# Kernel optimization log

Measured on AMD Instinct MI355X. Metric: run time of the kernel, lower is better.

Reference implementation:

```python
import jax, jax.numpy as jnp
import numpy as np

NEG_SLOPE = 0.2  # PyG GATConv default


def setup_inputs() -> dict:
    key = jax.random.key(0)
    k1, k2, k3, k4, k5, k6 = jax.random.split(key, 6)
    N, F_in, F_out, E = 50000, 512, 256, 400000
    x = jax.random.normal(k1, (N, F_in), dtype=jnp.float32)
    adj = jax.random.randint(k2, (2, E), 0, N, dtype=jnp.int64)  # [2, E] edge_index (src, dst)
    glorot = lambda k, shape: jax.random.uniform(
        k, shape, jnp.float32, -1.0, 1.0) * np.sqrt(6.0 / (shape[0] + shape[-1]))
    W = glorot(k3, (F_in, F_out))
    att_src = glorot(k4, (F_out,))
    att_dst = glorot(k5, (F_out,))
    bias = jnp.zeros((F_out,), dtype=jnp.float32)
    return {"x": x, "adj": adj, "W": W, "att_src": att_src, "att_dst": att_dst, "bias": bias}


def reference(x, adj, W, att_src, att_dst, bias):
    N = x.shape[0]
    # add self loops (PyG GATConv default add_self_loops=True)
    loops = jnp.arange(N, dtype=adj.dtype)
    src = jnp.concatenate([adj[0], loops])
    dst = jnp.concatenate([adj[1], loops])

    h = x @ W                          # [N, F_out] projected features
    a_src = h @ att_src                # [N] per-node source attention term
    a_dst = h @ att_dst                # [N]
    e = a_src[src] + a_dst[dst]        # [E+N] edge logits
    e = jnp.where(e > 0, e, NEG_SLOPE * e)  # leaky_relu

    # per-destination softmax over incoming edges (numerically stable)
    m = jax.ops.segment_max(e, dst, num_segments=N)
    ex = jnp.exp(e - m[dst])
    denom = jax.ops.segment_sum(ex, dst, num_segments=N)
    alpha = ex / denom[dst]            # [E+N]

    # weighted scatter-aggregate of source messages
    out = jax.ops.segment_sum(alpha[:, None] * h[src], dst, num_segments=N)
    out = out + bias
    return jax.nn.relu(out)
```

## Files before the change

### kernel.cpp

```cpp
#include <hip/hip_runtime.h>
#include <hip/hip_bf16.h>

typedef __attribute__((ext_vector_type(8))) short bf16x8;
typedef __attribute__((ext_vector_type(4))) float f32x4;
typedef unsigned short u16;

#define F_IN 512
#define F_OUT 256
#define NEG_SLOPE 0.2f

__device__ __forceinline__ float leaky(float e) { return e > 0.f ? e : NEG_SLOPE * e; }

__device__ __forceinline__ u16 f2bf(float x) {
    __hip_bfloat16 h = __float2bfloat16(x);
    return *reinterpret_cast<u16*>(&h);
}
__device__ __forceinline__ void bf2x2(unsigned p, float& a, float& b) {
    a = __uint_as_float(p << 16);
    b = __uint_as_float(p & 0xffff0000u);
}

__device__ __forceinline__ void dma16(const void* g, void* l) {
    __builtin_amdgcn_global_load_lds((const __attribute__((address_space(1))) void*)g,
                                     (__attribute__((address_space(3))) void*)l, 16, 0, 0);
}

__global__ void k_transpose(const float* __restrict__ W, u16* __restrict__ Wt) {
    int t = blockIdx.x * 256 + threadIdx.x;
    int k = t >> 8;
    int n = t & 255;
    Wt[n * F_IN + k] = f2bf(W[k * F_OUT + n]);
}

__global__ __launch_bounds__(256) void k_gemm(const float* __restrict__ X,
                                              const u16* __restrict__ Wt,
                                              u16* __restrict__ Hb, int N) {
    __shared__ float sA[128 * 32];
    __shared__ u16 sB[128 * 32];
    const int tid = threadIdx.x;
    const int wave = tid >> 6, lane = tid & 63;
    const int wm = (wave >> 1) * 64, wn = (wave & 1) * 64;
    const int tile_m = blockIdx.y * 128, tile_n = blockIdx.x * 128;

    f32x4 acc[4][4];
#pragma unroll
    for (int i = 0; i < 4; i++)
#pragma unroll
        for (int j = 0; j < 4; j++) acc[i][j] = (f32x4){0.f, 0.f, 0.f, 0.f};

    const int a_row_in = lane >> 3;
    const int a_gc = (lane & 7) ^ a_row_in;
    const int b_row_in = lane >> 2;
    const int b_gc = (lane & 3) ^ ((lane >> 3) & 3);

    for (int kb = 0; kb < F_IN / 32; ++kb) {
#pragma unroll
        for (int t = 0; t < 4; ++t) {
            int r0 = wave * 32 + t * 8;
            int grow = tile_m + r0 + a_row_in;
            if (grow >= N) grow = N - 1;
            dma16(&X[(size_t)grow * F_IN + kb * 32 + a_gc * 4], &sA[r0 * 32]);
        }
#pragma unroll
        for (int t = 0; t < 2; ++t) {
            int r0 = wave * 32 + t * 16;
            int grow = tile_n + r0 + b_row_in;
            dma16(&Wt[(size_t)grow * F_IN + kb * 32 + b_gc * 8], &sB[r0 * 32]);
        }
        __syncthreads();

        const int lm = lane & 15, q = lane >> 4;
        bf16x8 af[4], bfr[4];
#pragma unroll
        for (int i = 0; i < 4; i++) {
            const int arow = wm + i * 16 + lm;
            const int s7 = arow & 7;
            const float4 c0 = *(const float4*)&sA[arow * 32 + (((2 * q) ^ s7) << 2)];
            const float4 c1 = *(const float4*)&sA[arow * 32 + (((2 * q + 1) ^ s7) << 2)];
            u16 a8[8] = {f2bf(c0.x), f2bf(c0.y), f2bf(c0.z), f2bf(c0.w),
                         f2bf(c1.x), f2bf(c1.y), f2bf(c1.z), f2bf(c1.w)};
            af[i] = *(const bf16x8*)a8;
            const int brow = wn + i * 16 + lm;
            bfr[i] = *(const bf16x8*)&sB[brow * 32 + ((q ^ ((lm >> 1) & 3)) << 3)];
        }
#pragma unroll
        for (int i = 0; i < 4; i++)
#pragma unroll
            for (int j = 0; j < 4; j++)
                acc[i][j] = __builtin_amdgcn_mfma_f32_16x16x32_bf16(af[i], bfr[j], acc[i][j], 0, 0, 0);
        __syncthreads();
    }

    const int lc = lane & 15, lr4 = (lane >> 4) * 4;
    for (int i = 0; i < 4; i++)
        for (int j = 0; j < 4; j++) {
#pragma unroll
            for (int r = 0; r < 4; r++) {
                int row = tile_m + wm + i * 16 + lr4 + r;
                int col = tile_n + wn + j * 16 + lc;
                if (row < N) Hb[(size_t)row * F_OUT + col] = f2bf(acc[i][j][r]);
            }
        }
}

__global__ __launch_bounds__(256) void k_dots(const u16* __restrict__ Hb,
                                              const float* __restrict__ att_src,
                                              const float* __restrict__ att_dst,
                                              float* __restrict__ aS, float* __restrict__ aD,
                                              int* __restrict__ deg, int N) {
    int wave = threadIdx.x >> 6, lane = threadIdx.x & 63;
    int row = blockIdx.x * 4 + wave;
    if (row >= N) return;
    uint2 rv = *(const uint2*)&Hb[(size_t)row * F_OUT + lane * 4];
    float h0, h1, h2, h3;
    bf2x2(rv.x, h0, h1);
    bf2x2(rv.y, h2, h3);
    const float4 as = *(const float4*)&att_src[lane * 4];
    const float4 ad = *(const float4*)&att_dst[lane * 4];
    float s1 = h0 * as.x + h1 * as.y + h2 * as.z + h3 * as.w;
    float s2 = h0 * ad.x + h1 * ad.y + h2 * ad.z + h3 * ad.w;
    for (int off = 32; off; off >>= 1) {
        s1 += __shfl_down(s1, off);
        s2 += __shfl_down(s2, off);
    }
    if (lane == 0) {
        aS[row] = s1;
        aD[row] = s2;
        deg[row] = 0;
    }
}

__global__ void k_deg(const int* __restrict__ dsts, int* __restrict__ deg, int E) {
    int e = blockIdx.x * 256 + threadIdx.x;
    if (e >= E) return;
    atomicAdd(&deg[dsts[e]], 1);
}

__global__ __launch_bounds__(256) void k_scan1(const int* __restrict__ deg,
                                               int* __restrict__ bsum, int N) {
    __shared__ int ws[4];
    int t = threadIdx.x;
    int i = blockIdx.x * 256 + t;
    int v = (i < N) ? deg[i] : 0;
    for (int off = 32; off; off >>= 1) v += __shfl_down(v, off);
    if ((t & 63) == 0) ws[t >> 6] = v;
    __syncthreads();
    if (t == 0) bsum[blockIdx.x] = ws[0] + ws[1] + ws[2] + ws[3];
}

__global__ __launch_bounds__(256) void k_scan2(const int* __restrict__ bsum,
                                               int* __restrict__ boff, int* __restrict__ offs,
                                               int nb, int N) {
    __shared__ int ss[256];
    int t = threadIdx.x;
    int v = (t < nb) ? bsum[t] : 0;
    ss[t] = v;
    __syncthreads();
    for (int off = 1; off < 256; off <<= 1) {
        int u = (t >= off) ? ss[t - off] : 0;
        __syncthreads();
        ss[t] += u;
        __syncthreads();
    }
    boff[t] = ss[t] - v;
    if (t == 255) offs[N] = ss[255];
}

__global__ __launch_bounds__(256) void k_scan3(const int* __restrict__ deg,
                                               const int* __restrict__ boff,
                                               int* __restrict__ offs, int* __restrict__ cur,
                                               int N) {
    __shared__ int ss[256];
    int t = threadIdx.x;
    int i = blockIdx.x * 256 + t;
    int v = (i < N) ? deg[i] : 0;
    ss[t] = v;
    __syncthreads();
    for (int off = 1; off < 256; off <<= 1) {
        int u = (t >= off) ? ss[t - off] : 0;
        __syncthreads();
        ss[t] += u;
        __syncthreads();
    }
    int ex = ss[t] - v + boff[blockIdx.x];
    if (i < N) {
        offs[i] = ex;
        cur[i] = ex;
    }
}

__global__ void k_edge_scatter(const int* __restrict__ srcs, const int* __restrict__ dsts,
                               const float* __restrict__ aS, const float* __restrict__ aD,
                               int* __restrict__ cur, int* __restrict__ csrS,
                               float* __restrict__ csrW, int E) {
    int e = blockIdx.x * 256 + threadIdx.x;
    if (e >= E) return;
    int s = srcs[e], d = dsts[e];
    float ex = __expf(leaky(aS[s] + aD[d]));
    int pos = atomicAdd(&cur[d], 1);
    csrS[pos] = s;
    csrW[pos] = ex;
}

__global__ __launch_bounds__(256) void k_aggregate(const u16* __restrict__ Hb,
                                                   const float* __restrict__ aS,
                                                   const float* __restrict__ aD,
                                                   const int* __restrict__ offs,
                                                   const int* __restrict__ csrS,
                                                   const float* __restrict__ csrW,
                                                   const float* __restrict__ bias,
                                                   float* __restrict__ out, int N) {
    int wave = threadIdx.x >> 6, lane = threadIdx.x & 63;
    int i = blockIdx.x * 4 + wave;
    if (i >= N) return;
    float sex = __expf(leaky(aS[i] + aD[i]));

    uint2 rv = *(const uint2*)&Hb[(size_t)i * F_OUT + lane * 4];
    float f0, f1, f2, f3;
    bf2x2(rv.x, f0, f1);
    bf2x2(rv.y, f2, f3);
    float4 acc = {sex * f0, sex * f1, sex * f2, sex * f3};
    float wsum = sex;

    int beg = offs[i], end = offs[i + 1];
    int k = beg;
    for (; k + 4 <= end; k += 4) {
        int s0 = csrS[k], s1 = csrS[k + 1], s2 = csrS[k + 2], s3 = csrS[k + 3];
        float w0 = csrW[k], w1 = csrW[k + 1], w2 = csrW[k + 2], w3 = csrW[k + 3];
        uint2 g0 = *(const uint2*)&Hb[(size_t)s0 * F_OUT + lane * 4];
        uint2 g1 = *(const uint2*)&Hb[(size_t)s1 * F_OUT + lane * 4];
        uint2 g2 = *(const uint2*)&Hb[(size_t)s2 * F_OUT + lane * 4];
        uint2 g3 = *(const uint2*)&Hb[(size_t)s3 * F_OUT + lane * 4];
        wsum += w0 + w1 + w2 + w3;
        bf2x2(g0.x, f0, f1); bf2x2(g0.y, f2, f3);
        acc.x += w0 * f0; acc.y += w0 * f1; acc.z += w0 * f2; acc.w += w0 * f3;
        bf2x2(g1.x, f0, f1); bf2x2(g1.y, f2, f3);
        acc.x += w1 * f0; acc.y += w1 * f1; acc.z += w1 * f2; acc.w += w1 * f3;
        bf2x2(g2.x, f0, f1); bf2x2(g2.y, f2, f3);
        acc.x += w2 * f0; acc.y += w2 * f1; acc.z += w2 * f2; acc.w += w2 * f3;
        bf2x2(g3.x, f0, f1); bf2x2(g3.y, f2, f3);
        acc.x += w3 * f0; acc.y += w3 * f1; acc.z += w3 * f2; acc.w += w3 * f3;
    }
    for (; k < end; ++k) {
        int s = csrS[k];
        float w = csrW[k];
        uint2 r = *(const uint2*)&Hb[(size_t)s * F_OUT + lane * 4];
        wsum += w;
        bf2x2(r.x, f0, f1);
        bf2x2(r.y, f2, f3);
        acc.x += w * f0;
        acc.y += w * f1;
        acc.z += w * f2;
        acc.w += w * f3;
    }
    float inv = 1.f / wsum;
    const float4 bv = *(const float4*)&bias[lane * 4];
    float4 o;
    o.x = acc.x * inv + bv.x;
    o.y = acc.y * inv + bv.y;
    o.z = acc.z * inv + bv.z;
    o.w = acc.w * inv + bv.w;
    o.x = o.x > 0.f ? o.x : 0.f;
    o.y = o.y > 0.f ? o.y : 0.f;
    o.z = o.z > 0.f ? o.z : 0.f;
    o.w = o.w > 0.f ? o.w : 0.f;
    *(float4*)&out[(size_t)i * F_OUT + lane * 4] = o;
}

extern "C" void kernel_launch(void* const* d_in, const int* in_sizes, int n_in,
                              void* d_out, int out_size, void* d_ws, size_t ws_size,
                              hipStream_t stream) {
    const float* X = (const float*)d_in[0];
    const int* adj = (const int*)d_in[1];
    const float* W = (const float*)d_in[2];
    const float* att_src = (const float*)d_in[3];
    const float* att_dst = (const float*)d_in[4];
    const float* bias = (const float*)d_in[5];
    float* out = (float*)d_out;

    const int N = in_sizes[0] / F_IN;
    const int E = in_sizes[1] / 2;
    const int* srcs = adj;
    const int* dsts = adj + E;
    const int nb = (N + 255) / 256;

    char* p = (char*)d_ws;
    auto take = [&](size_t b) -> char* {
        char* q = p;
        p += (b + 255) & ~(size_t)255;
        return q;
    };
    u16* Hb = (u16*)take((size_t)N * F_OUT * sizeof(u16));
    u16* Wt = (u16*)take((size_t)F_IN * F_OUT * sizeof(u16));
    float* aS = (float*)take((size_t)N * sizeof(float));
    float* aD = (float*)take((size_t)N * sizeof(float));
    int* deg = (int*)take((size_t)N * sizeof(int));
    int* offs = (int*)take((size_t)(N + 1) * sizeof(int));
    int* cur = (int*)take((size_t)N * sizeof(int));
    int* bsum = (int*)take((size_t)256 * sizeof(int));
    int* boff = (int*)take((size_t)256 * sizeof(int));
    int* csrS = (int*)take((size_t)E * sizeof(int));
    float* csrW = (float*)take((size_t)E * sizeof(float));

    k_transpose<<<(F_IN * F_OUT) / 256, 256, 0, stream>>>(W, Wt);
    dim3 ggrid((F_OUT + 127) / 128, (N + 127) / 128);
    k_gemm<<<ggrid, 256, 0, stream>>>(X, Wt, Hb, N);
    k_dots<<<(N + 3) / 4, 256, 0, stream>>>(Hb, att_src, att_dst, aS, aD, deg, N);
    k_deg<<<(E + 255) / 256, 256, 0, stream>>>(dsts, deg, E);
    k_scan1<<<nb, 256, 0, stream>>>(deg, bsum, N);
    k_scan2<<<1, 256, 0, stream>>>(bsum, boff, offs, nb, N);
    k_scan3<<<nb, 256, 0, stream>>>(deg, boff, offs, cur, N);
    k_edge_scatter<<<(E + 255) / 256, 256, 0, stream>>>(srcs, dsts, aS, aD, cur, csrS, csrW, E);
    k_aggregate<<<(N + 3) / 4, 256, 0, stream>>>(Hb, aS, aD, offs, csrS, csrW, bias, out, N);
}
```

Before: 297.3 us.

## Double-buffer GEMM LDS loads and fuse attention dots into GEMM epilogue

The GEMM now stages tile kb+1 into a second LDS buffer via global_load_lds while computing tile kb, using explicit vmcnt waits and raw barriers instead of a load-then-sync loop. The separate k_dots kernel is removed: attention source/destination dot products are computed from fp32 accumulators in the GEMM epilogue, reduced across 16 lanes, and atomically added into aS/aD, which are zeroed (with deg) in the transpose kernel. This removes one kernel launch and a full reread of H, and hides global load latency. It doubles LDS use, which may lower occupancy, adds float atomics whose summation order is nondeterministic, and computes dots from fp32 rather than bf16-rounded values.

```diff
diff --git a/kernel.cpp b/kernel.cpp
--- a/kernel.cpp
+++ b/kernel.cpp
@@ -25,18 +25,29 @@
                                      (__attribute__((address_space(3))) void*)l, 16, 0, 0);
 }
 
-__global__ void k_transpose(const float* __restrict__ W, u16* __restrict__ Wt) {
+__global__ void k_transpose(const float* __restrict__ W, u16* __restrict__ Wt,
+                            float* __restrict__ aS, float* __restrict__ aD,
+                            int* __restrict__ deg, int N) {
     int t = blockIdx.x * 256 + threadIdx.x;
     int k = t >> 8;
     int n = t & 255;
     Wt[n * F_IN + k] = f2bf(W[k * F_OUT + n]);
+    if (t < N) {
+        aS[t] = 0.f;
+        aD[t] = 0.f;
+        deg[t] = 0;
+    }
 }
 
 __global__ __launch_bounds__(256) void k_gemm(const float* __restrict__ X,
                                               const u16* __restrict__ Wt,
-                                              u16* __restrict__ Hb, int N) {
-    __shared__ float sA[128 * 32];
-    __shared__ u16 sB[128 * 32];
+                                              const float* __restrict__ att_src,
+                                              const float* __restrict__ att_dst,
+                                              u16* __restrict__ Hb,
+                                              float* __restrict__ aS, float* __restrict__ aD,
+                                              int N) {
+    __shared__ float sA[2][128 * 32];
+    __shared__ u16 sB[2][128 * 32];
     const int tid = threadIdx.x;
     const int wave = tid >> 6, lane = tid & 63;
     const int wm = (wave >> 1) * 64, wn = (wave & 1) * 64;
@@ -53,46 +64,93 @@
     const int b_row_in = lane >> 2;
     const int b_gc = (lane & 3) ^ ((lane >> 3) & 3);
 
+    const float* aG[4];
+#pragma unroll
+    for (int t = 0; t < 4; ++t) {
+        int grow = tile_m + wave * 32 + t * 8 + a_row_in;
+        if (grow >= N) grow = N - 1;
+        aG[t] = &X[(size_t)grow * F_IN + a_gc * 4];
+    }
+    const u16* bG[2];
+#pragma unroll
+    for (int t = 0; t < 2; ++t) {
+        int grow = tile_n + wave * 32 + t * 16 + b_row_in;
+        bG[t] = &Wt[(size_t)grow * F_IN + b_gc * 8];
+    }
+
+    auto stage = [&](int kb, int buf) {
+#pragma unroll
+        for (int t = 0; t < 4; ++t)
+            dma16(aG[t] + kb * 32, &sA[buf][(wave * 32 + t * 8) * 32]);
+#pragma unroll
+        for (int t = 0; t < 2; ++t)
+            dma16(bG[t] + kb * 32, &sB[buf][(wave * 32 + t * 16) * 32]);
+    };
+
+    stage(0, 0);
+    int cur = 0;
+    const int lm = lane & 15, q = lane >> 4;
+
     for (int kb = 0; kb < F_IN / 32; ++kb) {
-#pragma unroll
-        for (int t = 0; t < 4; ++t) {
-            int r0 = wave * 32 + t * 8;
-            int grow = tile_m + r0 + a_row_in;
-            if (grow >= N) grow = N - 1;
-            dma16(&X[(size_t)grow * F_IN + kb * 32 + a_gc * 4], &sA[r0 * 32]);
+        if (kb + 1 < F_IN / 32) {
+            stage(kb + 1, cur ^ 1);
+            asm volatile("s_waitcnt vmcnt(6)" ::: "memory");
+        } else {
+            asm volatile("s_waitcnt vmcnt(0)" ::: "memory");
         }
-#pragma unroll
-        for (int t = 0; t < 2; ++t) {
-            int r0 = wave * 32 + t * 16;
-            int grow = tile_n + r0 + b_row_in;
-            dma16(&Wt[(size_t)grow * F_IN + kb * 32 + b_gc * 8], &sB[r0 * 32]);
-        }
-        __syncthreads();
-
-        const int lm = lane & 15, q = lane >> 4;
+        __builtin_amdgcn_sched_barrier(0);
+        __builtin_amdgcn_s_barrier();
+
         bf16x8 af[4], bfr[4];
 #pragma unroll
         for (int i = 0; i < 4; i++) {
             const int arow = wm + i * 16 + lm;
             const int s7 = arow & 7;
-            const float4 c0 = *(const float4*)&sA[arow * 32 + (((2 * q) ^ s7) << 2)];
-            const float4 c1 = *(const float4*)&sA[arow * 32 + (((2 * q + 1) ^ s7) << 2)];
+            const float4 c0 = *(const float4*)&sA[cur][arow * 32 + (((2 * q) ^ s7) << 2)];
+            const float4 c1 = *(const float4*)&sA[cur][arow * 32 + (((2 * q + 1) ^ s7) << 2)];
             u16 a8[8] = {f2bf(c0.x), f2bf(c0.y), f2bf(c0.z), f2bf(c0.w),
                          f2bf(c1.x), f2bf(c1.y), f2bf(c1.z), f2bf(c1.w)};
             af[i] = *(const bf16x8*)a8;
             const int brow = wn + i * 16 + lm;
-            bfr[i] = *(const bf16x8*)&sB[brow * 32 + ((q ^ ((lm >> 1) & 3)) << 3)];
+            bfr[i] = *(const bf16x8*)&sB[cur][brow * 32 + ((q ^ ((lm >> 1) & 3)) << 3)];
         }
 #pragma unroll
         for (int i = 0; i < 4; i++)
 #pragma unroll
             for (int j = 0; j < 4; j++)
                 acc[i][j] = __builtin_amdgcn_mfma_f32_16x16x32_bf16(af[i], bfr[j], acc[i][j], 0, 0, 0);
-        __syncthreads();
-    }
-
-    const int lc = lane & 15, lr4 = (lane >> 4) * 4;
-    for (int i = 0; i < 4; i++)
+        __builtin_amdgcn_s_barrier();
+        cur ^= 1;
+    }
+
+    const int lc = lm, lr4 = q * 4;
+    float vS[4], vD[4];
+#pragma unroll
+    for (int j = 0; j < 4; ++j) {
+        int col = tile_n + wn + j * 16 + lc;
+        vS[j] = att_src[col];
+        vD[j] = att_dst[col];
+    }
+#pragma unroll
+    for (int i = 0; i < 4; i++) {
+#pragma unroll
+        for (int r = 0; r < 4; r++) {
+            int row = tile_m + wm + i * 16 + lr4 + r;
+            float pS = acc[i][0][r] * vS[0] + acc[i][1][r] * vS[1] +
+                       acc[i][2][r] * vS[2] + acc[i][3][r] * vS[3];
+            float pD = acc[i][0][r] * vD[0] + acc[i][1][r] * vD[1] +
+                       acc[i][2][r] * vD[2] + acc[i][3][r] * vD[3];
+#pragma unroll
+            for (int off = 1; off < 16; off <<= 1) {
+                pS += __shfl_xor(pS, off);
+                pD += __shfl_xor(pD, off);
+            }
+            if (lc == 0 && row < N) {
+                atomicAdd(&aS[row], pS);
+                atomicAdd(&aD[row], pD);
+            }
+        }
+#pragma unroll
         for (int j = 0; j < 4; j++) {
 #pragma unroll
             for (int r = 0; r < 4; r++) {
@@ -101,32 +159,6 @@
                 if (row < N) Hb[(size_t)row * F_OUT + col] = f2bf(acc[i][j][r]);
             }
         }
-}
-
-__global__ __launch_bounds__(256) void k_dots(const u16* __restrict__ Hb,
-                                              const float* __restrict__ att_src,
-                                              const float* __restrict__ att_dst,
-                                              float* __restrict__ aS, float* __restrict__ aD,
-                                              int* __restrict__ deg, int N) {
-    int wave = threadIdx.x >> 6, lane = threadIdx.x & 63;
-    int row = blockIdx.x * 4 + wave;
-    if (row >= N) return;
-    uint2 rv = *(const uint2*)&Hb[(size_t)row * F_OUT + lane * 4];
-    float h0, h1, h2, h3;
-    bf2x2(rv.x, h0, h1);
-    bf2x2(rv.y, h2, h3);
-    const float4 as = *(const float4*)&att_src[lane * 4];
-    const float4 ad = *(const float4*)&att_dst[lane * 4];
-    float s1 = h0 * as.x + h1 * as.y + h2 * as.z + h3 * as.w;
-    float s2 = h0 * ad.x + h1 * ad.y + h2 * ad.z + h3 * ad.w;
-    for (int off = 32; off; off >>= 1) {
-        s1 += __shfl_down(s1, off);
-        s2 += __shfl_down(s2, off);
-    }
-    if (lane == 0) {
-        aS[row] = s1;
-        aD[row] = s2;
-        deg[row] = 0;
     }
 }
 
@@ -302,10 +334,9 @@
     int* csrS = (int*)take((size_t)E * sizeof(int));
     float* csrW = (float*)take((size_t)E * sizeof(float));
 
-    k_transpose<<<(F_IN * F_OUT) / 256, 256, 0, stream>>>(W, Wt);
+    k_transpose<<<(F_IN * F_OUT) / 256, 256, 0, stream>>>(W, Wt, aS, aD, deg, N);
     dim3 ggrid((F_OUT + 127) / 128, (N + 127) / 128);
-    k_gemm<<<ggrid, 256, 0, stream>>>(X, Wt, Hb, N);
-    k_dots<<<(N + 3) / 4, 256, 0, stream>>>(Hb, att_src, att_dst, aS, aD, deg, N);
+    k_gemm<<<ggrid, 256, 0, stream>>>(X, Wt, att_src, att_dst, Hb, aS, aD, N);
     k_deg<<<(E + 255) / 256, 256, 0, stream>>>(dsts, deg, E);
     k_scan1<<<nb, 256, 0, stream>>>(deg, bsum, N);
     k_scan2<<<1, 256, 0, stream>>>(bsum, boff, offs, nb, N);
```

After: 293.4 us. Within noise of the previous version (-1.3%).

## Load GEMM operands directly from global into MFMA fragments, drop LDS staging

Applied to the files above, without the earlier changes.

The GEMM kernel stops staging X and Wt tiles in shared memory through global_load_lds, and with them the two barriers per k-step. Each lane now reads its MFMA fragments straight from global memory, and the k-loop is fully unrolled. This relies on the caches to serve the repeated reads of rows across waves, giving up the explicit LDS reuse in exchange for no synchronisation. Separately, zeroing of the degree array moves from k_dots into k_transpose, which covers N because its grid has 131072 threads.

```diff
diff --git a/kernel.cpp b/kernel.cpp
--- a/kernel.cpp
+++ b/kernel.cpp
@@ -20,27 +20,37 @@
     b = __uint_as_float(p & 0xffff0000u);
 }
 
-__device__ __forceinline__ void dma16(const void* g, void* l) {
-    __builtin_amdgcn_global_load_lds((const __attribute__((address_space(1))) void*)g,
-                                     (__attribute__((address_space(3))) void*)l, 16, 0, 0);
-}
-
-__global__ void k_transpose(const float* __restrict__ W, u16* __restrict__ Wt) {
+__global__ void k_transpose(const float* __restrict__ W, u16* __restrict__ Wt,
+                            int* __restrict__ deg, int N) {
     int t = blockIdx.x * 256 + threadIdx.x;
     int k = t >> 8;
     int n = t & 255;
     Wt[n * F_IN + k] = f2bf(W[k * F_OUT + n]);
+    if (t < N) deg[t] = 0;
 }
 
 __global__ __launch_bounds__(256) void k_gemm(const float* __restrict__ X,
                                               const u16* __restrict__ Wt,
                                               u16* __restrict__ Hb, int N) {
-    __shared__ float sA[128 * 32];
-    __shared__ u16 sB[128 * 32];
     const int tid = threadIdx.x;
     const int wave = tid >> 6, lane = tid & 63;
     const int wm = (wave >> 1) * 64, wn = (wave & 1) * 64;
     const int tile_m = blockIdx.y * 128, tile_n = blockIdx.x * 128;
+    const int lm = lane & 15, q = lane >> 4;
+
+    const float* aP[4];
+#pragma unroll
+    for (int i = 0; i < 4; i++) {
+        int row = tile_m + wm + i * 16 + lm;
+        if (row >= N) row = N - 1;
+        aP[i] = &X[(size_t)row * F_IN + q * 8];
+    }
+    const u16* bP[4];
+#pragma unroll
+    for (int j = 0; j < 4; j++) {
+        int col = tile_n + wn + j * 16 + lm;
+        bP[j] = &Wt[(size_t)col * F_IN + q * 8];
+    }
 
     f32x4 acc[4][4];
 #pragma unroll
@@ -48,51 +58,31 @@
 #pragma unroll
         for (int j = 0; j < 4; j++) acc[i][j] = (f32x4){0.f, 0.f, 0.f, 0.f};
 
-    const int a_row_in = lane >> 3;
-    const int a_gc = (lane & 7) ^ a_row_in;
-    const int b_row_in = lane >> 2;
-    const int b_gc = (lane & 3) ^ ((lane >> 3) & 3);
-
+#pragma unroll
     for (int kb = 0; kb < F_IN / 32; ++kb) {
-#pragma unroll
-        for (int t = 0; t < 4; ++t) {
-            int r0 = wave * 32 + t * 8;
-            int grow = tile_m + r0 + a_row_in;
-            if (grow >= N) grow = N - 1;
-            dma16(&X[(size_t)grow * F_IN + kb * 32 + a_gc * 4], &sA[r0 * 32]);
-        }
-#pragma unroll
-        for (int t = 0; t < 2; ++t) {
-            int r0 = wave * 32 + t * 16;
-            int grow = tile_n + r0 + b_row_in;
-            dma16(&Wt[(size_t)grow * F_IN + kb * 32 + b_gc * 8], &sB[r0 * 32]);
-        }
-        __syncthreads();
-
-        const int lm = lane & 15, q = lane >> 4;
+        const int o = kb * 32;
         bf16x8 af[4], bfr[4];
 #pragma unroll
+        for (int j = 0; j < 4; j++) bfr[j] = *(const bf16x8*)(bP[j] + o);
+#pragma unroll
         for (int i = 0; i < 4; i++) {
-            const int arow = wm + i * 16 + lm;
-            const int s7 = arow & 7;
-            const float4 c0 = *(const float4*)&sA[arow * 32 + (((2 * q) ^ s7) << 2)];
-            const float4 c1 = *(const float4*)&sA[arow * 32 + (((2 * q + 1) ^ s7) << 2)];
+            const float4 c0 = *(const float4*)(aP[i] + o);
+            const float4 c1 = *(const float4*)(aP[i] + o + 4);
             u16 a8[8] = {f2bf(c0.x), f2bf(c0.y), f2bf(c0.z), f2bf(c0.w),
                          f2bf(c1.x), f2bf(c1.y), f2bf(c1.z), f2bf(c1.w)};
             af[i] = *(const bf16x8*)a8;
-            const int brow = wn + i * 16 + lm;
-            bfr[i] = *(const bf16x8*)&sB[brow * 32 + ((q ^ ((lm >> 1) & 3)) << 3)];
         }
 #pragma unroll
         for (int i = 0; i < 4; i++)
 #pragma unroll
             for (int j = 0; j < 4; j++)
                 acc[i][j] = __builtin_amdgcn_mfma_f32_16x16x32_bf16(af[i], bfr[j], acc[i][j], 0, 0, 0);
-        __syncthreads();
-    }
-
-    const int lc = lane & 15, lr4 = (lane >> 4) * 4;
+    }
+
+    const int lc = lm, lr4 = q * 4;
+#pragma unroll
     for (int i = 0; i < 4; i++)
+#pragma unroll
         for (int j = 0; j < 4; j++) {
 #pragma unroll
             for (int r = 0; r < 4; r++) {
@@ -107,7 +97,7 @@
                                               const float* __restrict__ att_src,
                                               const float* __restrict__ att_dst,
                                               float* __restrict__ aS, float* __restrict__ aD,
-                                              int* __restrict__ deg, int N) {
+                                              int N) {
     int wave = threadIdx.x >> 6, lane = threadIdx.x & 63;
     int row = blockIdx.x * 4 + wave;
     if (row >= N) return;
@@ -126,7 +116,6 @@
     if (lane == 0) {
         aS[row] = s1;
         aD[row] = s2;
-        deg[row] = 0;
     }
 }
 
@@ -302,10 +291,10 @@
     int* csrS = (int*)take((size_t)E * sizeof(int));
     float* csrW = (float*)take((size_t)E * sizeof(float));
 
-    k_transpose<<<(F_IN * F_OUT) / 256, 256, 0, stream>>>(W, Wt);
+    k_transpose<<<(F_IN * F_OUT) / 256, 256, 0, stream>>>(W, Wt, deg, N);
     dim3 ggrid((F_OUT + 127) / 128, (N + 127) / 128);
     k_gemm<<<ggrid, 256, 0, stream>>>(X, Wt, Hb, N);
-    k_dots<<<(N + 3) / 4, 256, 0, stream>>>(Hb, att_src, att_dst, aS, aD, deg, N);
+    k_dots<<<(N + 3) / 4, 256, 0, stream>>>(Hb, att_src, att_dst, aS, aD, N);
     k_deg<<<(E + 255) / 256, 256, 0, stream>>>(dsts, deg, E);
     k_scan1<<<nb, 256, 0, stream>>>(deg, bsum, N);
     k_scan2<<<1, 256, 0, stream>>>(bsum, boff, offs, nb, N);
```

Result: slower. 345.8 us (+16.3%).
